# Kernel tuning notes

Hardware: AMD Instinct MI355X
Metric: run time of the kernel (lower is better)

Reference implementation:

```python
import jax, jax.numpy as jnp
import numpy as np
from jax import lax

SAMPLING_FRACTION = 0.5
BIG = 1e8  # initial 'infinite' distance, matches torch's 1e8


def _farthest_point_sample(points, init_idx, n_sample):
    """points: (B,N,C) float; init_idx: (B,) int. Returns (B, n_sample) int32 indices."""
    B, N, C = points.shape
    batch = jnp.arange(B)

    def step(carry, _):
        distances, farthest = carry            # (B,N), (B,)
        centroid = points[batch, farthest]     # (B,C)
        d = jnp.sum((points - centroid[:, None, :]) ** 2, axis=-1)  # (B,N) squared euclid
        distances = jnp.minimum(distances, d)
        new_farthest = jnp.argmax(distances, axis=-1)
        return (distances, new_farthest), farthest  # record index BEFORE update (matches torch)

    init = (jnp.full((B, N), BIG, dtype=points.dtype), init_idx.astype(jnp.int32))
    _, centroids = lax.scan(step, init, None, length=n_sample)
    return centroids.T  # (B, n_sample)


def _index_points(x, idx):
    # x: (B, N, ...) ; idx: (B, M) -> (B, M, ...)
    return jnp.take_along_axis(x, idx.reshape(idx.shape + (1,) * (x.ndim - 2)), axis=1) if x.ndim > 2 else jnp.take_along_axis(x, idx, axis=1)


def setup_inputs() -> dict:
    key = jax.random.key(0)
    k1, k2, k3 = jax.random.split(key, 3)
    B, N, C, D = 16, 8192, 3, 256
    coords = jax.random.normal(k1, (B, N, C), dtype=jnp.float32)
    values = jax.random.normal(k2, (B, N, D), dtype=jnp.float32)
    mask = jnp.ones((B, N), dtype=jnp.float32)
    init_idx = jax.random.randint(k3, (B,), 0, N)
    return {"coords": coords, "values": values, "mask": mask, "init_idx": init_idx}


def reference(coords, values, mask, init_idx):
    B, N, C = coords.shape
    n_sample = int(round(N * SAMPLING_FRACTION))
    idx = _farthest_point_sample(coords, init_idx, n_sample)  # (B, n_sample)
    query_coords = _index_points(coords, idx)  # (B, M, C)
    query_values = _index_points(values, idx)  # (B, M, D)
    query_mask = _index_points(mask, idx)      # (B, M)
    return (query_coords, query_values, query_mask)
```

## Files before the change

### kernel.cpp

```cpp
#include <hip/hip_runtime.h>

typedef unsigned long long u64;
typedef float v2f __attribute__((ext_vector_type(2)));

#define FPS_N   8192
#define FPS_M   (FPS_N / 2)
#define FPS_T   256
#define FPS_W   (FPS_T / 64)
#define FPS_PPT (FPS_N / FPS_T)
#define FPS_PR  (FPS_PPT / 2)

__device__ __forceinline__ v2f pk_add(v2f a, v2f b) {
    v2f r; asm("v_pk_add_f32 %0, %1, %2" : "=v"(r) : "v"(a), "v"(b)); return r;
}
__device__ __forceinline__ v2f pk_mul(v2f a, v2f b) {
    v2f r; asm("v_pk_mul_f32 %0, %1, %2" : "=v"(r) : "v"(a), "v"(b)); return r;
}
__device__ __forceinline__ v2f pk_fma(v2f a, v2f b, v2f c) {
    v2f r; asm("v_pk_fma_f32 %0, %1, %2, %3" : "=v"(r) : "v"(a), "v"(b), "v"(c)); return r;
}

template<int CTRL>
__device__ __forceinline__ float dpp_max_step(float x) {
    int s = __builtin_amdgcn_update_dpp(0, __float_as_int(x), CTRL, 0xf, 0xf, true);
    return fmaxf(x, __int_as_float(s));
}
__device__ __forceinline__ float wave_max_nn(float x) {
    x = dpp_max_step<0x111>(x);
    x = dpp_max_step<0x112>(x);
    x = dpp_max_step<0x114>(x);
    x = dpp_max_step<0x118>(x);
    x = dpp_max_step<0x142>(x);
    x = dpp_max_step<0x143>(x);
    return __int_as_float(__builtin_amdgcn_readlane(__float_as_int(x), 63));
}
__device__ __forceinline__ float readlane_f(float x, int l) {
    return __int_as_float(__builtin_amdgcn_readlane(__float_as_int(x), l));
}

__global__ __launch_bounds__(FPS_T, 1) void fps_kernel(
    const float* __restrict__ coords,
    const int*   __restrict__ init_idx,
    int*         __restrict__ out_idx,
    int M)
{
    __shared__ float sx[FPS_N], sy[FPS_N], sz[FPS_N];
    __shared__ int   hist[FPS_M];
    __shared__ float swd[2][FPS_W];
    __shared__ int   swi[2][FPS_W];

    const int b    = blockIdx.x;
    const int tid  = threadIdx.x;
    const int lane = tid & 63;
    const int wv   = tid >> 6;
    const float* cb = coords + (size_t)b * FPS_N * 3;

    float f[96];
    const float4* cb4 = reinterpret_cast<const float4*>(cb);
    #pragma unroll
    for (int i = 0; i < 24; ++i) {
        float4 v = cb4[tid * 24 + i];
        f[i*4+0] = v.x; f[i*4+1] = v.y; f[i*4+2] = v.z; f[i*4+3] = v.w;
    }

    v2f px[FPS_PR], py[FPS_PR], pz[FPS_PR], dist[FPS_PR];
    const int base = tid * FPS_PPT;
    #pragma unroll
    for (int k = 0; k < FPS_PPT; ++k) {
        sx[base+k] = f[3*k+0]; sy[base+k] = f[3*k+1]; sz[base+k] = f[3*k+2];
    }
    #pragma unroll
    for (int j = 0; j < FPS_PR; ++j) {
        px[j] = v2f{f[6*j+0], f[6*j+3]};
        py[j] = v2f{f[6*j+1], f[6*j+4]};
        pz[j] = v2f{f[6*j+2], f[6*j+5]};
        dist[j] = v2f{1e8f, 1e8f};
    }
    __syncthreads();

    int far = init_idx[b];
    float cx = sx[far], cy = sy[far], cz = sz[far];

    for (int s = 0; s < M; ++s) {
        if (tid == 0) hist[s] = far;

        const v2f ncx = v2f{-cx, -cx};
        const v2f ncy = v2f{-cy, -cy};
        const v2f ncz = v2f{-cz, -cz};
        float pm[FPS_PR];
        float m = 0.0f;
        #pragma unroll
        for (int j = 0; j < FPS_PR; ++j) {
            v2f dx2 = pk_add(px[j], ncx);
            v2f dy2 = pk_add(py[j], ncy);
            v2f dz2 = pk_add(pz[j], ncz);
            v2f d2  = pk_fma(dz2, dz2, pk_fma(dy2, dy2, pk_mul(dx2, dx2)));
            v2f nd;
            nd.x = fminf(dist[j].x, d2.x);
            nd.y = fminf(dist[j].y, d2.y);
            dist[j] = nd;
            pm[j] = fmaxf(nd.x, nd.y);
            m = fmaxf(m, pm[j]);
        }
        int jw = 0;
        #pragma unroll
        for (int j = FPS_PR - 1; j >= 0; --j)
            jw = (pm[j] == m) ? j : jw;
        float dxh = pm[0];
        #pragma unroll
        for (int j = 0; j < FPS_PR; ++j)
            dxh = (j == jw) ? dist[j].x : dxh;
        int myidx = base + 2 * jw + ((dxh == m) ? 0 : 1);

        float wm = wave_max_nn(m);
        u64 ball = __ballot(m == wm);
        int fl   = (int)__builtin_ctzll(ball);
        int widx = __builtin_amdgcn_readlane(myidx, fl);

        const int par = s & 1;
        if (lane == 0) {
            swd[par][wv] = wm;
            swi[par][wv] = widx;
        }
        __syncthreads();

        float cand = swd[par][lane & (FPS_W - 1)];
        int   cidx = swi[par][lane & (FPS_W - 1)];
        float fx = sx[cidx], fy = sy[cidx], fz = sz[cidx];
        float g = cand;
        g = dpp_max_step<0x111>(g);
        g = dpp_max_step<0x112>(g);
        float gm = readlane_f(g, 3);
        u64 b2 = __ballot(cand == gm);
        int l2 = (int)__builtin_ctzll(b2);
        far = __builtin_amdgcn_readlane(cidx, l2);
        cx  = readlane_f(fx, l2);
        cy  = readlane_f(fy, l2);
        cz  = readlane_f(fz, l2);
    }

    __syncthreads();
    int4* ob = reinterpret_cast<int4*>(out_idx + (size_t)b * M);
    const int4* hb = reinterpret_cast<const int4*>(hist);
    for (int i = tid; i < M / 4; i += FPS_T) ob[i] = hb[i];
}

__global__ void gather_kernel(
    const float* __restrict__ coords,
    const float* __restrict__ values,
    const float* __restrict__ mask,
    const int*   __restrict__ idx,
    float* __restrict__ out_coords,
    float* __restrict__ out_values,
    float* __restrict__ out_mask,
    int N, int M, int D)
{
    const int bm = blockIdx.x;
    const int b  = bm / M;
    const int m  = bm - b * M;
    const int j  = idx[bm];
    const int l  = threadIdx.x;

    const float4* src = reinterpret_cast<const float4*>(values + ((size_t)b * N + j) * D);
    float4*       dst = reinterpret_cast<float4*>(out_values + ((size_t)b * M + m) * D);
    dst[l] = src[l];

    if (l < 3) {
        out_coords[((size_t)b * M + m) * 3 + l] = coords[((size_t)b * N + j) * 3 + l];
    } else if (l == 3) {
        out_mask[(size_t)b * M + m] = mask[(size_t)b * N + j];
    }
}

extern "C" void kernel_launch(void* const* d_in, const int* in_sizes, int n_in,
                              void* d_out, int out_size, void* d_ws, size_t ws_size,
                              hipStream_t stream)
{
    const float* coords   = (const float*)d_in[0];
    const float* values   = (const float*)d_in[1];
    const float* mask     = (const float*)d_in[2];
    const int*   init_idx = (const int*)d_in[3];

    const int B = in_sizes[3];
    const int N = in_sizes[2] / B;
    const int D = in_sizes[1] / (B * N);
    const int M = N / 2;

    float* out_coords = (float*)d_out;
    float* out_values = out_coords + (size_t)B * M * 3;
    float* out_mask   = out_values + (size_t)B * M * D;

    int* idx = (int*)d_ws;

    fps_kernel<<<B, FPS_T, 0, stream>>>(coords, init_idx, idx, M);
    gather_kernel<<<B * M, D / 4, 0, stream>>>(coords, values, mask, idx,
                                               out_coords, out_values, out_mask,
                                               N, M, D);
}
```

Baseline: 4.019 ms.

## Replace per-step barrier with tagged LDS flag exchange and double threads in FPS

Raises the FPS block from 256 to 512 threads, halving the points each thread holds. The per-iteration __syncthreads is replaced by lock-free exchange: each wave publishes its max distance, index and winning coordinates as 64-bit words tagged with the step number, and all waves spin until every slot carries the current tag. The LDS history array becomes a per-thread register buffer written straight to global memory at the end. The aim is to shorten the serial per-step latency of the 4096-step loop, at the cost of more waves spinning on LDS and a dependence on relaxed atomic ordering and tag packing being correct.

```diff
diff --git a/kernel.cpp b/kernel.cpp
--- a/kernel.cpp
+++ b/kernel.cpp
@@ -5,10 +5,11 @@
 
 #define FPS_N   8192
 #define FPS_M   (FPS_N / 2)
-#define FPS_T   256
+#define FPS_T   512
 #define FPS_W   (FPS_T / 64)
 #define FPS_PPT (FPS_N / FPS_T)
 #define FPS_PR  (FPS_PPT / 2)
+#define FPS_IPT (FPS_M / FPS_T)
 
 __device__ __forceinline__ v2f pk_add(v2f a, v2f b) {
     v2f r; asm("v_pk_add_f32 %0, %1, %2" : "=v"(r) : "v"(a), "v"(b)); return r;
@@ -45,9 +46,8 @@
     int M)
 {
     __shared__ float sx[FPS_N], sy[FPS_N], sz[FPS_N];
-    __shared__ int   hist[FPS_M];
-    __shared__ float swd[2][FPS_W];
-    __shared__ int   swi[2][FPS_W];
+    __shared__ u64 mkey[2][FPS_W];
+    __shared__ u64 mc0[2][FPS_W], mc1[2][FPS_W], mc2[2][FPS_W];
 
     const int b    = blockIdx.x;
     const int tid  = threadIdx.x;
@@ -55,11 +55,16 @@
     const int wv   = tid >> 6;
     const float* cb = coords + (size_t)b * FPS_N * 3;
 
-    float f[96];
+    if (tid < 2 * FPS_W) {
+        ((u64*)mkey)[tid] = 0ull;
+        ((u64*)mc0)[tid] = 0ull; ((u64*)mc1)[tid] = 0ull; ((u64*)mc2)[tid] = 0ull;
+    }
+
+    float f[48];
     const float4* cb4 = reinterpret_cast<const float4*>(cb);
     #pragma unroll
-    for (int i = 0; i < 24; ++i) {
-        float4 v = cb4[tid * 24 + i];
+    for (int i = 0; i < 12; ++i) {
+        float4 v = cb4[tid * 12 + i];
         f[i*4+0] = v.x; f[i*4+1] = v.y; f[i*4+2] = v.z; f[i*4+3] = v.w;
     }
 
@@ -81,68 +86,107 @@
     int far = init_idx[b];
     float cx = sx[far], cy = sy[far], cz = sz[far];
 
-    for (int s = 0; s < M; ++s) {
-        if (tid == 0) hist[s] = far;
-
-        const v2f ncx = v2f{-cx, -cx};
-        const v2f ncy = v2f{-cy, -cy};
-        const v2f ncz = v2f{-cz, -cz};
-        float pm[FPS_PR];
-        float m = 0.0f;
+    int buf[FPS_IPT];
+    #pragma unroll
+    for (int i = 0; i < FPS_IPT; ++i) buf[i] = 0;
+
+    for (int so = 0; so < M; so += FPS_IPT) {
+        const int owner = so >> 3;
         #pragma unroll
-        for (int j = 0; j < FPS_PR; ++j) {
-            v2f dx2 = pk_add(px[j], ncx);
-            v2f dy2 = pk_add(py[j], ncy);
-            v2f dz2 = pk_add(pz[j], ncz);
-            v2f d2  = pk_fma(dz2, dz2, pk_fma(dy2, dy2, pk_mul(dx2, dx2)));
-            v2f nd;
-            nd.x = fminf(dist[j].x, d2.x);
-            nd.y = fminf(dist[j].y, d2.y);
-            dist[j] = nd;
-            pm[j] = fmaxf(nd.x, nd.y);
-            m = fmaxf(m, pm[j]);
+        for (int si = 0; si < FPS_IPT; ++si) {
+            const int s = so + si;
+            if (tid == owner) buf[si] = far;
+
+            const v2f ncx = v2f{-cx, -cx};
+            const v2f ncy = v2f{-cy, -cy};
+            const v2f ncz = v2f{-cz, -cz};
+            float pm[FPS_PR];
+            float m = 0.0f;
+            #pragma unroll
+            for (int j = 0; j < FPS_PR; ++j) {
+                v2f dx2 = pk_add(px[j], ncx);
+                v2f dy2 = pk_add(py[j], ncy);
+                v2f dz2 = pk_add(pz[j], ncz);
+                v2f d2  = pk_fma(dz2, dz2, pk_fma(dy2, dy2, pk_mul(dx2, dx2)));
+                v2f nd;
+                nd.x = fminf(dist[j].x, d2.x);
+                nd.y = fminf(dist[j].y, d2.y);
+                dist[j] = nd;
+                pm[j] = fmaxf(nd.x, nd.y);
+                m = fmaxf(m, pm[j]);
+            }
+            int jw = 0;
+            #pragma unroll
+            for (int j = FPS_PR - 1; j >= 0; --j)
+                jw = (pm[j] == m) ? j : jw;
+            float dxh = pm[0];
+            #pragma unroll
+            for (int j = 0; j < FPS_PR; ++j)
+                dxh = (j == jw) ? dist[j].x : dxh;
+            int myidx = base + 2 * jw + ((dxh == m) ? 0 : 1);
+
+            float fx = sx[myidx], fy = sy[myidx], fz = sz[myidx];
+
+            float wm = wave_max_nn(m);
+            u64 ball = __ballot(m == wm);
+            int fl   = (int)__builtin_ctzll(ball);
+            int widx = __builtin_amdgcn_readlane(myidx, fl);
+            float wcx = readlane_f(fx, fl);
+            float wcy = readlane_f(fy, fl);
+            float wcz = readlane_f(fz, fl);
+
+            const int par = s & 1;
+            const unsigned tag = (unsigned)(s + 1);
+            if (lane == 0) {
+                u64 key = ((u64)(unsigned)__float_as_uint(wm) << 32)
+                        | ((u64)(unsigned)widx << 13) | (u64)tag;
+                __hip_atomic_store(&mkey[par][wv], key,
+                                   __ATOMIC_RELAXED, __HIP_MEMORY_SCOPE_WORKGROUP);
+                __hip_atomic_store(&mc0[par][wv],
+                    ((u64)(unsigned)__float_as_uint(wcx) << 32) | (u64)tag,
+                    __ATOMIC_RELAXED, __HIP_MEMORY_SCOPE_WORKGROUP);
+                __hip_atomic_store(&mc1[par][wv],
+                    ((u64)(unsigned)__float_as_uint(wcy) << 32) | (u64)tag,
+                    __ATOMIC_RELAXED, __HIP_MEMORY_SCOPE_WORKGROUP);
+                __hip_atomic_store(&mc2[par][wv],
+                    ((u64)(unsigned)__float_as_uint(wcz) << 32) | (u64)tag,
+                    __ATOMIC_RELAXED, __HIP_MEMORY_SCOPE_WORKGROUP);
+            }
+
+            const int sl = lane & (FPS_W - 1);
+            u64 k, c0, c1, c2;
+            do {
+                k  = __hip_atomic_load(&mkey[par][sl], __ATOMIC_RELAXED, __HIP_MEMORY_SCOPE_WORKGROUP);
+                c0 = __hip_atomic_load(&mc0[par][sl],  __ATOMIC_RELAXED, __HIP_MEMORY_SCOPE_WORKGROUP);
+                c1 = __hip_atomic_load(&mc1[par][sl],  __ATOMIC_RELAXED, __HIP_MEMORY_SCOPE_WORKGROUP);
+                c2 = __hip_atomic_load(&mc2[par][sl],  __ATOMIC_RELAXED, __HIP_MEMORY_SCOPE_WORKGROUP);
+            } while (!__all(((unsigned)(k & 0x1FFFull) == tag) &
+                            ((unsigned)(c0 & 0xFFFFFFFFull) == tag) &
+                            ((unsigned)(c1 & 0xFFFFFFFFull) == tag) &
+                            ((unsigned)(c2 & 0xFFFFFFFFull) == tag)));
+
+            float cand = __int_as_float((int)(k >> 32));
+            int   cidx = (int)((k >> 13) & 0x1FFF);
+            float gx = __int_as_float((int)(c0 >> 32));
+            float gy = __int_as_float((int)(c1 >> 32));
+            float gz = __int_as_float((int)(c2 >> 32));
+            float g = cand;
+            g = dpp_max_step<0x111>(g);
+            g = dpp_max_step<0x112>(g);
+            g = dpp_max_step<0x114>(g);
+            float gm = readlane_f(g, 7);
+            u64 b2 = __ballot(cand == gm);
+            int l2 = (int)__builtin_ctzll(b2);
+            far = __builtin_amdgcn_readlane(cidx, l2);
+            cx  = readlane_f(gx, l2);
+            cy  = readlane_f(gy, l2);
+            cz  = readlane_f(gz, l2);
         }
-        int jw = 0;
-        #pragma unroll
-        for (int j = FPS_PR - 1; j >= 0; --j)
-            jw = (pm[j] == m) ? j : jw;
-        float dxh = pm[0];
-        #pragma unroll
-        for (int j = 0; j < FPS_PR; ++j)
-            dxh = (j == jw) ? dist[j].x : dxh;
-        int myidx = base + 2 * jw + ((dxh == m) ? 0 : 1);
-
-        float wm = wave_max_nn(m);
-        u64 ball = __ballot(m == wm);
-        int fl   = (int)__builtin_ctzll(ball);
-        int widx = __builtin_amdgcn_readlane(myidx, fl);
-
-        const int par = s & 1;
-        if (lane == 0) {
-            swd[par][wv] = wm;
-            swi[par][wv] = widx;
-        }
-        __syncthreads();
-
-        float cand = swd[par][lane & (FPS_W - 1)];
-        int   cidx = swi[par][lane & (FPS_W - 1)];
-        float fx = sx[cidx], fy = sy[cidx], fz = sz[cidx];
-        float g = cand;
-        g = dpp_max_step<0x111>(g);
-        g = dpp_max_step<0x112>(g);
-        float gm = readlane_f(g, 3);
-        u64 b2 = __ballot(cand == gm);
-        int l2 = (int)__builtin_ctzll(b2);
-        far = __builtin_amdgcn_readlane(cidx, l2);
-        cx  = readlane_f(fx, l2);
-        cy  = readlane_f(fy, l2);
-        cz  = readlane_f(fz, l2);
-    }
-
-    __syncthreads();
-    int4* ob = reinterpret_cast<int4*>(out_idx + (size_t)b * M);
-    const int4* hb = reinterpret_cast<const int4*>(hist);
-    for (int i = tid; i < M / 4; i += FPS_T) ob[i] = hb[i];
+    }
+
+    int4* ob = reinterpret_cast<int4*>(out_idx + (size_t)b * M + tid * FPS_IPT);
+    ob[0] = int4{buf[0], buf[1], buf[2], buf[3]};
+    ob[1] = int4{buf[4], buf[5], buf[6], buf[7]};
 }
 
 __global__ void gather_kernel(
```

After: 4.070 ms. Within noise of the previous version (+1.3%).
